# Performance work log

Measured on AMD Instinct MI355X. Metric: run time of the kernel, lower is better.

## Reference

```python
import jax, jax.numpy as jnp
import numpy as np

L, F, LOG_T, NMIN, NMAX = 16, 2, 19, 16, 2048
T = 2 ** LOG_T
N_ROWS = 524288
PRIMES = np.array([1, 2654435761, 805459861], dtype=np.uint32)
# 8 corner offsets of the unit cube, bits (dx, dy, dz)
CORNERS = np.stack(np.meshgrid([0, 1], [0, 1], [0, 1], indexing='ij'), axis=-1).reshape(8, 3)


def setup_inputs() -> dict:
    key = jax.random.key(0)
    k1, k2 = jax.random.split(key)
    x = jax.random.uniform(k1, (N_ROWS, 3), dtype=jnp.float32)  # coords in [0,1)
    hashmap = jax.random.normal(k2, (L, F, T), dtype=jnp.float32) * 1e-2
    growth = np.exp((np.log(NMAX) - np.log(NMIN)) / (L - 1))
    resolution = jnp.asarray(np.floor(NMIN * growth ** np.arange(L)), dtype=jnp.float32)
    return {"x": x, "hashmap": hashmap, "resolution": resolution}


def _hash_encode(x, hashmap, resolution):
    # x: [n, 3], hashmap: [L, F, T], resolution: [L]
    n = x.shape[0]
    xs = x[:, None, :] * resolution[None, :, None]          # [n, L, 3]
    x0f = jnp.floor(xs)
    frac = xs - x0f                                          # trilinear fracs [n, L, 3]
    x0 = x0f.astype(jnp.uint32)

    primes = jnp.asarray(PRIMES)                             # [3] uint32
    h0 = x0 * primes                                         # [n, L, 3] (wraps mod 2^32)
    h1 = (x0 + jnp.uint32(1)) * primes                       # [n, L, 3]
    hpair = jnp.stack([h0, h1], axis=-2)                     # [n, L, 2, 3]

    c = jnp.asarray(CORNERS, dtype=jnp.int32)                # [8, 3]
    # hashed index per corner: xor of per-dim hashes, masked to table size
    idx = (hpair[:, :, c[:, 0], 0]
           ^ hpair[:, :, c[:, 1], 1]
           ^ hpair[:, :, c[:, 2], 2]) & jnp.uint32(T - 1)    # [n, L, 8]

    wpair = jnp.stack([1.0 - frac, frac], axis=-2)           # [n, L, 2, 3]
    w = (wpair[:, :, c[:, 0], 0]
         * wpair[:, :, c[:, 1], 1]
         * wpair[:, :, c[:, 2], 2])                          # [n, L, 8]

    def per_level(hm_l, idx_l, w_l):
        # hm_l: [F, T], idx_l: [n, 8], w_l: [n, 8]
        feats = jnp.take(hm_l, idx_l, axis=1)                # [F, n, 8]
        return jnp.einsum('fnc,nc->nf', feats, w_l)          # [n, F]

    out = jax.vmap(per_level)(hashmap,
                              idx.transpose(1, 0, 2),
                              w.transpose(1, 0, 2))          # [L, n, F]
    # match torch layout: (L,F,n) -> (n, L, F) -> (n, L*F)
    return out.transpose(1, 0, 2).reshape(n, L * F)


def reference(x, hashmap, resolution):
    return _hash_encode(x, hashmap, resolution)
```

## Files before the change

kernel.cpp:

```cpp
#include <hip/hip_runtime.h>
#include <hip/hip_fp16.h>


#define HG_L     16
#define HG_LOG_T 19
#define HG_T     (1u << HG_LOG_T)
#define HG_N     524288u
#define HP1      2654435761u
#define HP2      805459861u

#define DS0 17u
#define DS1 23u
#define DS2 31u
#define DS3 43u
#define DS4 59u
#define DS5 81u
#define DOFF0 0u
#define DOFF1 4913u
#define DOFF2 17080u
#define DOFF3 46871u
#define DOFF4 126378u
#define DOFF5 331757u
#define DTOTAL 863198u

#define TAB_BYTES ((size_t)10u * HG_T * 4u)

#define NB_INTER 5120u
#define NB_OCT   6744u

__device__ __forceinline__ unsigned pack_h2(float f0, float f1) {
    __half2 h = __floats2half2_rn(f0, f1);
    return *reinterpret_cast<unsigned*>(&h);
}

__global__ __launch_bounds__(256) void hg_prep(
    const float* __restrict__ hm,
    __half2* __restrict__ wst,
    uint4* __restrict__ oct)
{
    const unsigned bid = blockIdx.x;
    const unsigned M = HG_T - 1u;
    if (bid < NB_INTER) {
        const unsigned u  = (bid * 256u + threadIdx.x) * 4u;
        const unsigned l6 = u >> HG_LOG_T;
        const unsigned t  = u & M;
        const float* base = hm + (size_t)(l6 + 6u) * (2u * HG_T);
        const float4 a = *reinterpret_cast<const float4*>(base + t);
        const float4 b = *reinterpret_cast<const float4*>(base + HG_T + t);
        uint4 o;
        o.x = pack_h2(a.x, b.x);
        o.y = pack_h2(a.y, b.y);
        o.z = pack_h2(a.z, b.z);
        o.w = pack_h2(a.w, b.w);
        *reinterpret_cast<uint4*>(wst + u) = o;
        return;
    }
    const unsigned j = (bid - NB_INTER) * 256u + threadIdx.x;
    if (j >= 2u * DTOTAL) return;
    const unsigned cell = j >> 1;
    const unsigned zh   = j & 1u;
    unsigned l, S, off;
    if      (cell < DOFF1) { l = 0; S = DS0; off = DOFF0; }
    else if (cell < DOFF2) { l = 1; S = DS1; off = DOFF1; }
    else if (cell < DOFF3) { l = 2; S = DS2; off = DOFF2; }
    else if (cell < DOFF4) { l = 3; S = DS3; off = DOFF3; }
    else if (cell < DOFF5) { l = 4; S = DS4; off = DOFF4; }
    else                   { l = 5; S = DS5; off = DOFF5; }
    const unsigned i  = cell - off;
    const unsigned x  = i % S;
    const unsigned t1 = i / S;
    const unsigned y  = t1 % S;
    const unsigned z  = t1 / S + zh;
    const unsigned hz = z * HP2;
    const unsigned hy0 = y * HP1, hy1 = hy0 + HP1;
    const unsigned i00 = (hy0 ^ hz ^ x) & M;
    const unsigned i10 = (hy0 ^ hz ^ (x + 1u)) & M;
    const unsigned i01 = (hy1 ^ hz ^ x) & M;
    const unsigned i11 = (hy1 ^ hz ^ (x + 1u)) & M;
    const float* b0 = hm + (size_t)l * (2u * HG_T);
    uint4 o;
    o.x = pack_h2(b0[i00], b0[i00 + HG_T]);
    o.y = pack_h2(b0[i10], b0[i10 + HG_T]);
    o.z = pack_h2(b0[i01], b0[i01 + HG_T]);
    o.w = pack_h2(b0[i11], b0[i11 + HG_T]);
    oct[j] = o;
}

__device__ __forceinline__ float2 hfv(unsigned raw) {
    return __half22float2(*reinterpret_cast<const __half2*>(&raw));
}

__device__ __forceinline__ unsigned sel4(const uint4& g, unsigned k) {
    const unsigned lo = (k & 1u) ? g.y : g.x;
    const unsigned hi = (k & 1u) ? g.w : g.z;
    return (k & 2u) ? hi : lo;
}

template <unsigned S, unsigned OFF>
__device__ __forceinline__ float2 enc_dense(
    float px, float py, float pz, float res,
    const uint4* __restrict__ oct)
{
    const float xs0 = px * res, xs1 = py * res, xs2 = pz * res;
    const float fl0 = floorf(xs0), fl1 = floorf(xs1), fl2 = floorf(xs2);
    const float fr0 = xs0 - fl0, fr1 = xs1 - fl1, fr2 = xs2 - fl2;
    const unsigned x0 = (unsigned)fl0;
    const unsigned y0 = (unsigned)fl1;
    const unsigned z0 = (unsigned)fl2;

    const unsigned i = ((z0 * S + y0) * S + x0 + OFF) * 2u;
    const uint4 q0 = oct[i];
    const uint4 q1 = oct[i + 1u];

    const float w0x = 1.0f - fr0, w1x = fr0;
    const float w0y = 1.0f - fr1, w1y = fr1;
    const float w0z = 1.0f - fr2, w1z = fr2;

    const float2 a00 = hfv(q0.x), a10 = hfv(q0.y), a01 = hfv(q0.z), a11 = hfv(q0.w);
    const float2 b00 = hfv(q1.x), b10 = hfv(q1.y), b01 = hfv(q1.z), b11 = hfv(q1.w);

    const float s0x = w0y * (w0x * a00.x + w1x * a10.x) + w1y * (w0x * a01.x + w1x * a11.x);
    const float s0y = w0y * (w0x * a00.y + w1x * a10.y) + w1y * (w0x * a01.y + w1x * a11.y);
    const float s1x = w0y * (w0x * b00.x + w1x * b10.x) + w1y * (w0x * b01.x + w1x * b11.x);
    const float s1y = w0y * (w0x * b00.y + w1x * b10.y) + w1y * (w0x * b01.y + w1x * b11.y);

    return make_float2(w0z * s0x + w1z * s1x, w0z * s0y + w1z * s1y);
}

__device__ __forceinline__ float2 enc_hash(
    float px, float py, float pz, float res,
    const uint2* __restrict__ tab2)
{
    const float xs0 = px * res, xs1 = py * res, xs2 = pz * res;
    const float fl0 = floorf(xs0), fl1 = floorf(xs1), fl2 = floorf(xs2);
    const float fr0 = xs0 - fl0, fr1 = xs1 - fl1, fr2 = xs2 - fl2;
    const unsigned x0 = (unsigned)fl0;
    const unsigned y0 = (unsigned)fl1;
    const unsigned z0 = (unsigned)fl2;
    const unsigned M = HG_T - 1u;
    const uint4* tab4 = reinterpret_cast<const uint4*>(tab2);

    const unsigned hy0 = y0 * HP1, hy1 = hy0 + HP1;
    const unsigned hz0 = z0 * HP2, hz1 = hz0 + HP2;
    const unsigned H0 = hy0 ^ hz0;
    const unsigned H1 = hy1 ^ hz0;
    const unsigned H2 = hy0 ^ hz1;
    const unsigned H3 = hy1 ^ hz1;
    const unsigned x1 = x0 + 1u;

    const unsigned i00 = (H0 ^ x0) & M, i01 = (H0 ^ x1) & M;
    const unsigned i10 = (H1 ^ x0) & M, i11 = (H1 ^ x1) & M;
    const unsigned i20 = (H2 ^ x0) & M, i21 = (H2 ^ x1) & M;
    const unsigned i30 = (H3 ^ x0) & M, i31 = (H3 ^ x1) & M;

    const uint4 g0 = tab4[i00 >> 2];
    const uint4 g1 = tab4[i10 >> 2];
    const uint4 g2 = tab4[i20 >> 2];
    const uint4 g3 = tab4[i30 >> 2];

    unsigned c00 = sel4(g0, i00 & 3u), c01 = sel4(g0, i01 & 3u);
    unsigned c10 = sel4(g1, i10 & 3u), c11 = sel4(g1, i11 & 3u);
    unsigned c20 = sel4(g2, i20 & 3u), c21 = sel4(g2, i21 & 3u);
    unsigned c30 = sel4(g3, i30 & 3u), c31 = sel4(g3, i31 & 3u);

    if ((x0 & 3u) == 3u) {
        { const uint2 p = tab2[i01 >> 1]; c01 = (i01 & 1u) ? p.y : p.x; }
        { const uint2 p = tab2[i11 >> 1]; c11 = (i11 & 1u) ? p.y : p.x; }
        { const uint2 p = tab2[i21 >> 1]; c21 = (i21 & 1u) ? p.y : p.x; }
        { const uint2 p = tab2[i31 >> 1]; c31 = (i31 & 1u) ? p.y : p.x; }
    }

    const float w0x = 1.0f - fr0, w1x = fr0;
    const float w00 = (1.0f - fr1) * (1.0f - fr2);
    const float w10 = fr1 * (1.0f - fr2);
    const float w01 = (1.0f - fr1) * fr2;
    const float w11 = fr1 * fr2;

    float ax = 0.0f, ay = 0.0f;
    { const float2 v0 = hfv(c00), v1 = hfv(c01);
      ax += w00 * (w0x * v0.x + w1x * v1.x);
      ay += w00 * (w0x * v0.y + w1x * v1.y); }
    { const float2 v0 = hfv(c10), v1 = hfv(c11);
      ax += w10 * (w0x * v0.x + w1x * v1.x);
      ay += w10 * (w0x * v0.y + w1x * v1.y); }
    { const float2 v0 = hfv(c20), v1 = hfv(c21);
      ax += w01 * (w0x * v0.x + w1x * v1.x);
      ay += w01 * (w0x * v0.y + w1x * v1.y); }
    { const float2 v0 = hfv(c30), v1 = hfv(c31);
      ax += w11 * (w0x * v0.x + w1x * v1.x);
      ay += w11 * (w0x * v0.y + w1x * v1.y); }
    return make_float2(ax, ay);
}

__global__ __launch_bounds__(256, 4) void hg_main(
    const float* __restrict__ x,
    const uint2* __restrict__ tab2,
    const uint4* __restrict__ oct,
    const float* __restrict__ resolution,
    float*       __restrict__ out)
{
    const unsigned tid = threadIdx.x;
    const unsigned p0  = blockIdx.x * 512u + tid;
    const unsigned p1  = p0 + 256u;
    const float ax0 = x[p0 * 3 + 0], ay0 = x[p0 * 3 + 1], az0 = x[p0 * 3 + 2];
    const float ax1 = x[p1 * 3 + 0], ay1 = x[p1 * 3 + 1], az1 = x[p1 * 3 + 2];
    float4* d0 = reinterpret_cast<float4*>(out + (size_t)p0 * 32u);
    float4* d1 = reinterpret_cast<float4*>(out + (size_t)p1 * 32u);

#define HPAIR(L0)                                                              \
    {                                                                          \
        const uint2* t0 = tab2 + (size_t)((L0) - 6) * (HG_T / 2u);             \
        const uint2* t1 = tab2 + (size_t)((L0) - 5) * (HG_T / 2u);             \
        const float r0 = resolution[(L0)], r1 = resolution[(L0) + 1];          \
        const float2 a0 = enc_hash(ax0, ay0, az0, r0, t0);                     \
        const float2 b0 = enc_hash(ax0, ay0, az0, r1, t1);                     \
        const float2 a1 = enc_hash(ax1, ay1, az1, r0, t0);                     \
        const float2 b1 = enc_hash(ax1, ay1, az1, r1, t1);                     \
        d0[3 + ((L0) - 6) / 2] = make_float4(a0.x, a0.y, b0.x, b0.y);          \
        d1[3 + ((L0) - 6) / 2] = make_float4(a1.x, a1.y, b1.x, b1.y);          \
        __syncthreads();                                                       \
    }
    HPAIR(6)
    HPAIR(8)
    HPAIR(10)
    HPAIR(12)
    HPAIR(14)
#undef HPAIR

    {
        const float r0 = resolution[0], r1 = resolution[1];
        const float2 a0 = enc_dense<DS0, DOFF0>(ax0, ay0, az0, r0, oct);
        const float2 b0 = enc_dense<DS1, DOFF1>(ax0, ay0, az0, r1, oct);
        const float2 a1 = enc_dense<DS0, DOFF0>(ax1, ay1, az1, r0, oct);
        const float2 b1 = enc_dense<DS1, DOFF1>(ax1, ay1, az1, r1, oct);
        d0[0] = make_float4(a0.x, a0.y, b0.x, b0.y);
        d1[0] = make_float4(a1.x, a1.y, b1.x, b1.y);
        __syncthreads();
    }
    {
        const float r2 = resolution[2], r3 = resolution[3];
        const float2 a0 = enc_dense<DS2, DOFF2>(ax0, ay0, az0, r2, oct);
        const float2 b0 = enc_dense<DS3, DOFF3>(ax0, ay0, az0, r3, oct);
        const float2 a1 = enc_dense<DS2, DOFF2>(ax1, ay1, az1, r2, oct);
        const float2 b1 = enc_dense<DS3, DOFF3>(ax1, ay1, az1, r3, oct);
        d0[1] = make_float4(a0.x, a0.y, b0.x, b0.y);
        d1[1] = make_float4(a1.x, a1.y, b1.x, b1.y);
        __syncthreads();
    }
    {
        const float r4 = resolution[4], r5 = resolution[5];
        const float2 a0 = enc_dense<DS4, DOFF4>(ax0, ay0, az0, r4, oct);
        const float2 b0 = enc_dense<DS5, DOFF5>(ax0, ay0, az0, r5, oct);
        const float2 a1 = enc_dense<DS4, DOFF4>(ax1, ay1, az1, r4, oct);
        const float2 b1 = enc_dense<DS5, DOFF5>(ax1, ay1, az1, r5, oct);
        d0[2] = make_float4(a0.x, a0.y, b0.x, b0.y);
        d1[2] = make_float4(a1.x, a1.y, b1.x, b1.y);
    }
}

extern "C" void kernel_launch(void* const* d_in, const int* in_sizes, int n_in,
                              void* d_out, int out_size, void* d_ws, size_t ws_size,
                              hipStream_t stream) {
    const float* x          = (const float*)d_in[0];
    const float* hashmap    = (const float*)d_in[1];
    const float* resolution = (const float*)d_in[2];
    float* out              = (float*)d_out;

    __half2* wst = (__half2*)d_ws;
    uint4*   oct = (uint4*)((char*)d_ws + TAB_BYTES);
    const uint2* tab2 = (const uint2*)d_ws;

    hipLaunchKernelGGL(hg_prep, dim3(NB_INTER + NB_OCT), dim3(256), 0, stream,
                       hashmap, wst, oct);

    hipLaunchKernelGGL(hg_main, dim3(HG_N / 512u), dim3(256), 0, stream,
                       x, tab2, oct, resolution, out);
}
```

Before: 419.2 us.

## Replace block-level syncs with soft grid-wide barriers between level phases

Swaps the per-level __syncthreads in the main kernel for a grid-wide spin barrier on an atomic counter, which the prep kernel resets. The aim is to keep every block on the same hash level at the same time, so the working set of table gathers stays small and hits in L2. The barrier falls back after a spin limit if the 1024 blocks are not all resident. The atomic spin loop and sleep add overhead and a risk of stalls, and two dense-level phases are merged under one barrier.

```diff
diff --git a/kernel.cpp b/kernel.cpp
--- a/kernel.cpp
+++ b/kernel.cpp
@@ -24,9 +24,11 @@
 #define DTOTAL 863198u
 
 #define TAB_BYTES ((size_t)10u * HG_T * 4u)
+#define OCT_BYTES ((size_t)DTOTAL * 32u)
 
 #define NB_INTER 5120u
 #define NB_OCT   6744u
+#define NBLK_MAIN 1024u
 
 __device__ __forceinline__ unsigned pack_h2(float f0, float f1) {
     __half2 h = __floats2half2_rn(f0, f1);
@@ -36,10 +38,12 @@
 __global__ __launch_bounds__(256) void hg_prep(
     const float* __restrict__ hm,
     __half2* __restrict__ wst,
-    uint4* __restrict__ oct)
+    uint4* __restrict__ oct,
+    unsigned* __restrict__ bar)
 {
     const unsigned bid = blockIdx.x;
     const unsigned M = HG_T - 1u;
+    if (bid == 0 && threadIdx.x == 0) *bar = 0u;
     if (bid < NB_INTER) {
         const unsigned u  = (bid * 256u + threadIdx.x) * 4u;
         const unsigned l6 = u >> HG_LOG_T;
@@ -192,12 +196,37 @@
     return make_float2(ax, ay);
 }
 
+__device__ __forceinline__ bool soft_grid_barrier(
+    unsigned* bar, unsigned gen, bool enabled)
+{
+    __shared__ int ok_s;
+    __syncthreads();
+    if (threadIdx.x == 0) {
+        __hip_atomic_fetch_add(bar, 1u, __ATOMIC_ACQ_REL,
+                               __HIP_MEMORY_SCOPE_AGENT);
+        int ok = 1;
+        if (enabled) {
+            const unsigned target = gen * NBLK_MAIN;
+            int spins = 0;
+            while (__hip_atomic_load(bar, __ATOMIC_ACQUIRE,
+                                     __HIP_MEMORY_SCOPE_AGENT) < target) {
+                __builtin_amdgcn_s_sleep(8);
+                if (++spins > 2000) { ok = 0; break; }
+            }
+        }
+        ok_s = ok;
+    }
+    __syncthreads();
+    return ok_s != 0;
+}
+
 __global__ __launch_bounds__(256, 4) void hg_main(
     const float* __restrict__ x,
     const uint2* __restrict__ tab2,
     const uint4* __restrict__ oct,
     const float* __restrict__ resolution,
-    float*       __restrict__ out)
+    float*       __restrict__ out,
+    unsigned*    __restrict__ bar)
 {
     const unsigned tid = threadIdx.x;
     const unsigned p0  = blockIdx.x * 512u + tid;
@@ -206,6 +235,9 @@
     const float ax1 = x[p1 * 3 + 0], ay1 = x[p1 * 3 + 1], az1 = x[p1 * 3 + 2];
     float4* d0 = reinterpret_cast<float4*>(out + (size_t)p0 * 32u);
     float4* d1 = reinterpret_cast<float4*>(out + (size_t)p1 * 32u);
+
+    bool sync_ok = true;
+    unsigned gen = 0;
 
 #define HPAIR(L0)                                                              \
     {                                                                          \
@@ -218,7 +250,7 @@
         const float2 b1 = enc_hash(ax1, ay1, az1, r1, t1);                     \
         d0[3 + ((L0) - 6) / 2] = make_float4(a0.x, a0.y, b0.x, b0.y);          \
         d1[3 + ((L0) - 6) / 2] = make_float4(a1.x, a1.y, b1.x, b1.y);          \
-        __syncthreads();                                                       \
+        sync_ok = soft_grid_barrier(bar, ++gen, sync_ok);                      \
     }
     HPAIR(6)
     HPAIR(8)
@@ -235,17 +267,14 @@
         const float2 b1 = enc_dense<DS1, DOFF1>(ax1, ay1, az1, r1, oct);
         d0[0] = make_float4(a0.x, a0.y, b0.x, b0.y);
         d1[0] = make_float4(a1.x, a1.y, b1.x, b1.y);
-        __syncthreads();
-    }
-    {
         const float r2 = resolution[2], r3 = resolution[3];
-        const float2 a0 = enc_dense<DS2, DOFF2>(ax0, ay0, az0, r2, oct);
-        const float2 b0 = enc_dense<DS3, DOFF3>(ax0, ay0, az0, r3, oct);
-        const float2 a1 = enc_dense<DS2, DOFF2>(ax1, ay1, az1, r2, oct);
-        const float2 b1 = enc_dense<DS3, DOFF3>(ax1, ay1, az1, r3, oct);
-        d0[1] = make_float4(a0.x, a0.y, b0.x, b0.y);
-        d1[1] = make_float4(a1.x, a1.y, b1.x, b1.y);
-        __syncthreads();
+        const float2 c0 = enc_dense<DS2, DOFF2>(ax0, ay0, az0, r2, oct);
+        const float2 e0 = enc_dense<DS3, DOFF3>(ax0, ay0, az0, r3, oct);
+        const float2 c1 = enc_dense<DS2, DOFF2>(ax1, ay1, az1, r2, oct);
+        const float2 e1 = enc_dense<DS3, DOFF3>(ax1, ay1, az1, r3, oct);
+        d0[1] = make_float4(c0.x, c0.y, e0.x, e0.y);
+        d1[1] = make_float4(c1.x, c1.y, e1.x, e1.y);
+        sync_ok = soft_grid_barrier(bar, ++gen, sync_ok);
     }
     {
         const float r4 = resolution[4], r5 = resolution[5];
@@ -266,13 +295,14 @@
     const float* resolution = (const float*)d_in[2];
     float* out              = (float*)d_out;
 
-    __half2* wst = (__half2*)d_ws;
-    uint4*   oct = (uint4*)((char*)d_ws + TAB_BYTES);
+    __half2*  wst = (__half2*)d_ws;
+    uint4*    oct = (uint4*)((char*)d_ws + TAB_BYTES);
+    unsigned* bar = (unsigned*)((char*)d_ws + TAB_BYTES + OCT_BYTES);
     const uint2* tab2 = (const uint2*)d_ws;
 
     hipLaunchKernelGGL(hg_prep, dim3(NB_INTER + NB_OCT), dim3(256), 0, stream,
-                       hashmap, wst, oct);
-
-    hipLaunchKernelGGL(hg_main, dim3(HG_N / 512u), dim3(256), 0, stream,
-                       x, tab2, oct, resolution, out);
-}
+                       hashmap, wst, oct, bar);
+
+    hipLaunchKernelGGL(hg_main, dim3(NBLK_MAIN), dim3(256), 0, stream,
+                       x, tab2, oct, resolution, out, bar);
+}
```

Result: slower. 1.301 ms (+210.3%).
